# Optimization experiments

Measured on AMD Instinct MI355X. Metric: run time of the kernel, lower is better.

The kernel has to match this reference:

```python
import jax, jax.numpy as jnp
import numpy as np

B, T, U, N, K, H, O = 64, 800, 64, 64, 10, 512, 121
CLIP_LSTM, CLIP_OUT = 10.0, 100.0


def setup_inputs() -> dict:
    key = jax.random.key(0)
    ks = jax.random.split(key, 16)
    s = 0.08
    return {
        "strokes": jax.random.normal(ks[0], (B, T, 3), jnp.float32),
        "transcriptions": jax.random.uniform(ks[1], (B, U, N), jnp.float32),
        "W0": jax.random.normal(ks[2], (3 + N, 4 * H), jnp.float32) * s,
        "R0": jax.random.normal(ks[3], (H, 4 * H), jnp.float32) * s,
        "b0": jnp.zeros((4 * H,), jnp.float32),
        "Wd": jax.random.normal(ks[4], (H, 3 * K), jnp.float32) * 0.01,
        "bd": jnp.zeros((3 * K,), jnp.float32),
        "W1": jax.random.normal(ks[5], (H + N + 3, 4 * H), jnp.float32) * s,
        "R1": jax.random.normal(ks[6], (H, 4 * H), jnp.float32) * s,
        "b1": jnp.zeros((4 * H,), jnp.float32),
        "W2": jax.random.normal(ks[7], (H + N + 3, 4 * H), jnp.float32) * s,
        "R2": jax.random.normal(ks[8], (H, 4 * H), jnp.float32) * s,
        "b2": jnp.zeros((4 * H,), jnp.float32),
        "Wo": jax.random.normal(ks[9], (3 * H, O), jnp.float32) * s,
        "bo": jnp.zeros((O,), jnp.float32),
    }


def _lstm_step(h, c, z):
    i, f, g, o = jnp.split(z, 4, axis=-1)
    c2 = jax.nn.sigmoid(f) * c + jax.nn.sigmoid(i) * jnp.tanh(g)
    h2 = jax.nn.sigmoid(o) * jnp.tanh(c2)
    return h2, c2


def _lstm_layer(x_seq, W, R, b):
    # x_seq: [T, B, D] -> hidden sequence [T, B, H]
    xz = jnp.einsum('tbd,dh->tbh', x_seq, W) + b  # precompute input projections

    def step(carry, xz_t):
        h, c = carry
        h2, c2 = _lstm_step(h, c, xz_t + h @ R)
        return (h2, c2), h2

    z0 = jnp.zeros((x_seq.shape[1], R.shape[0]), x_seq.dtype)
    _, hs = jax.lax.scan(step, (z0, z0), xz)
    return hs


def _make_clipper(cv):
    @jax.custom_vjp
    def f(y):
        return y
    f.defvjp(lambda y: (y, None), lambda _, dy: (jnp.clip(dy, -cv, cv),))
    return f


_clip_lstm = _make_clipper(CLIP_LSTM)
_clip_out = _make_clipper(CLIP_OUT)


def _forward(strokes, transcriptions, W0, R0, b0, Wd, bd, W1, R1, b1, W2, R2, b2, Wo, bo):
    idx = jnp.arange(1, U + 2, dtype=strokes.dtype)  # enumerated char positions [U+1]
    x_t = jnp.swapaxes(strokes, 0, 1)  # [T, B, 3]

    def step(carry, x):
        w, kappa, h, c = carry
        z = jnp.concatenate([x, w], axis=-1) @ W0 + h @ R0 + b0
        h2, c2 = _lstm_step(h, c, z)
        y = jnp.exp(h2 @ Wd + bd).reshape(-1, 3, K)  # [B, 3, K]
        alpha, beta, dk = y[:, 0], y[:, 1], y[:, 2]
        kappa2 = kappa + dk  # [B, K]
        # Gaussian window over U+1 positions, summed over K mixtures
        phi = alpha[..., None] * jnp.exp(-beta[..., None] * (kappa2[..., None] - idx) ** 2)
        wfull = phi.sum(axis=1)  # [B, U+1]
        att = jnp.argmax(wfull, axis=-1).astype(strokes.dtype)  # [B]
        w2 = jnp.einsum('bu,bun->bn', wfull[:, :U], transcriptions)  # soft window [B, N]
        return (w2, kappa2, h2, c2), (h2, w2, att)

    zf = lambda d: jnp.zeros((B, d), strokes.dtype)
    init = (zf(N), zf(K), zf(H), zf(H))
    _, (h0_seq, w_seq, att_seq) = jax.lax.scan(step, init, x_t)

    x1 = jnp.concatenate([_clip_lstm(h0_seq), w_seq, x_t], axis=-1)  # [T, B, H+N+3]
    h1_seq = _lstm_layer(x1, W1, R1, b1)
    x2 = jnp.concatenate([_clip_lstm(h1_seq), w_seq, x_t], axis=-1)
    h2_seq = _lstm_layer(x2, W2, R2, b2)
    hall = jnp.concatenate([h0_seq, h1_seq, h2_seq], axis=-1)  # [T, B, 3H]
    out = _clip_out(hall @ Wo + bo)
    return jnp.swapaxes(out, 0, 1), jnp.swapaxes(att_seq, 0, 1)  # [B,T,O], [B,T]


def reference(strokes, transcriptions, W0, R0, b0, Wd, bd, W1, R1, b1, W2, R2, b2, Wo, bo):
    return _forward(strokes, transcriptions, W0, R0, b0, Wd, bd, W1, R1, b1, W2, R2, b2, Wo, bo)
```

## Files before the change

kernel.cpp:

```cpp
#include <hip/hip_runtime.h>

#define B_   64
#define T_   800
#define U_   64
#define N_   64
#define KMIX 10
#define H_   512
#define O_   121
#define C4_  2048

#define NB_L0  64
#define NB_L1  64
#define NB_L2  64
#define NB_OUT 8
#define NB_ATT 4
#define NBLK  (NB_L0 + NB_L1 + NB_L2 + NB_OUT + NB_ATT)
#define NTHR  1024
#define RING  8
#define RB    (RING - 1)
#define FS    8

#define AL(pp) __hip_atomic_load((pp), __ATOMIC_RELAXED, __HIP_MEMORY_SCOPE_AGENT)

struct Params {
  const float* strokes; const float* transcr;
  const float* W0; const float* b0;
  const float* bd;
  const float* W1; const float* b1;
  const float* W2; const float* b2;
  const float* bo;
  const float4* PR0; const float4* PW0w;
  const float4* PH1; const float4* PR1; const float4* PW1w;
  const float4* PH2; const float4* PR2; const float4* PW2w;
  const float4* PWo; const float4* PWd;
  float* h0r; float* h1r; float* h2r;
  float* wr;
  int *h0f, *h1f, *h2f, *wfl, *outf;
  float* outp; float* attp;
};

__device__ __forceinline__ float sigf(float x) { return 1.0f / (1.0f + expf(-x)); }

__device__ __forceinline__ double f32q(double x) {
  double ax = fabs(x);
  if (ax >= 0x1p-126) return (double)(float)x;
  return rint(x * 0x1p149) * 0x1p-149;
}

__device__ __forceinline__ void cstoref(float* p, float v) {
  __hip_atomic_store(p, v, __ATOMIC_RELAXED, __HIP_MEMORY_SCOPE_AGENT);
}

__device__ __forceinline__ int* FP(int* arr, int tt, int bq) {
  return arr + ((size_t)tt * 8 + bq) * FS;
}
__device__ __forceinline__ void waitflag(const int* f, int target) {
  while (__hip_atomic_load(f, __ATOMIC_RELAXED, __HIP_MEMORY_SCOPE_AGENT) < target)
    __builtin_amdgcn_s_sleep(1);
}
__device__ __forceinline__ void postflag(int* f) {
  __hip_atomic_fetch_add(f, 1, __ATOMIC_RELAXED, __HIP_MEMORY_SCOPE_AGENT);
}

__device__ __forceinline__ void stage4k(float* dstL, const float* src, int t) {
  const double* s = (const double*)src;
  double v0 = AL(s + t), v1 = AL(s + 1024 + t);
  double* d = (double*)dstL;
  d[t] = v0; d[1024 + t] = v1;
}
__device__ __forceinline__ void stage4k2(float* d1, const float* s1,
                                         float* d2, const float* s2, int t) {
  const double* a = (const double*)s1;
  const double* b = (const double*)s2;
  double a0 = AL(a + t), a1 = AL(a + 1024 + t);
  double b0 = AL(b + t), b1 = AL(b + 1024 + t);
  double* dA = (double*)d1; dA[t] = a0; dA[1024 + t] = a1;
  double* dB = (double*)d2; dB[t] = b0; dB[1024 + t] = b1;
}
__device__ __forceinline__ void stage512(float* dstL, const float* src, int t) {
  if (t < 256) {
    double v = AL((const double*)src + t);
    ((double*)dstL)[t] = v;
  }
}

__device__ __forceinline__ void dot4gl(const float* Xl,
                                       const float4* __restrict__ W,
                                       int k4, int col, float acc[4]) {
  const float4* X = (const float4*)Xl;
  #pragma unroll 2
  for (int kk = 0; kk < k4; ++kk) {
    float4 xv = X[kk];
    #pragma unroll
    for (int g = 0; g < 4; ++g) {
      float4 wv = W[kk * C4_ + g * H_ + col];
      acc[g] = fmaf(xv.x, wv.x, acc[g]);
      acc[g] = fmaf(xv.y, wv.y, acc[g]);
      acc[g] = fmaf(xv.z, wv.z, acc[g]);
      acc[g] = fmaf(xv.w, wv.w, acc[g]);
    }
  }
}

__device__ __forceinline__ float dot1l(const float* Xl,
                                       const float4* __restrict__ W,
                                       int k4, int stride) {
  const float4* X = (const float4*)Xl;
  float a = 0.0f;
  #pragma unroll 4
  for (int kk = 0; kk < k4; ++kk) {
    float4 xv = X[kk];
    float4 wv = W[kk * stride];
    a = fmaf(xv.x, wv.x, a); a = fmaf(xv.y, wv.y, a);
    a = fmaf(xv.z, wv.z, a); a = fmaf(xv.w, wv.w, a);
  }
  return a;
}

__global__ void pack_k(const float* __restrict__ src, float* __restrict__ dst,
                       int K, int C, int ld) {
  int idx = blockIdx.x * 256 + threadIdx.x;
  if (idx >= K * C) return;
  int k = idx / C, c = idx - k * C;
  dst[(size_t)(k >> 2) * C * 4 + (size_t)c * 4 + (k & 3)] = src[(size_t)k * ld + c];
}

__global__ __launch_bounds__(NTHR, 4)
void net_kernel(Params p) {
  const int q = blockIdx.x;
  const int t = threadIdx.x;

  __shared__ float  s_buf[12288];
  __shared__ float  s_y[16][32];
  __shared__ float  s_k2[16][10];
  __shared__ float  s_kap[16][10];
  __shared__ double s_wf[16][66];

  if (q < NB_L0) {
    const int bq = q >> 3, colg = q & 7;
    const int kh = t >> 9;
    const int bl = (t >> 6) & 7, cl = t & 63;
    const int b = bq * 8 + bl, col = colg * 64 + cl;
    float* sh = s_buf;
    float* sw = s_buf + 4096;
    float4* s_red = (float4*)(s_buf + 4608);
    float creg = 0.0f;
    for (int i = 0; i < T_; ++i) {
      if (t == 0) {
        if (i >= 1) waitflag(FP(p.h0f, i - 1, bq), 8);
        if (i >= 8) waitflag(FP(p.outf, i - 8, bq), 1);
      }
      __syncthreads();
      const int slp = (i - 1) & RB;
      stage4k(sh, &p.h0r[((size_t)slp * B_ + bq * 8) * H_], t);
      float acc[4] = {0.f, 0.f, 0.f, 0.f};
      if (kh == 0) {
        const float* xs = &p.strokes[(b * T_ + i) * 3];
        float x0 = xs[0], x1 = xs[1], x2 = xs[2];
        #pragma unroll
        for (int g = 0; g < 4; ++g) {
          int cg = g * H_ + col;
          acc[g] = p.b0[cg] + x0 * p.W0[cg] + x1 * p.W0[C4_ + cg] + x2 * p.W0[2 * C4_ + cg];
        }
      }
      __syncthreads();
      dot4gl(sh + bl * H_ + kh * 256, p.PR0 + (size_t)kh * 64 * C4_, 64, col, acc);
      if (t == 0 && i >= 1) waitflag(FP(p.wfl, i - 1, bq), 1);
      __syncthreads();
      stage512(sw, &p.wr[((size_t)slp * B_ + bq * 8) * N_], t);
      __syncthreads();
      dot4gl(sw + bl * N_ + kh * 32, p.PW0w + (size_t)kh * 8 * C4_, 8, col, acc);
      if (kh) { float4 r; r.x = acc[0]; r.y = acc[1]; r.z = acc[2]; r.w = acc[3]; s_red[t - 512] = r; }
      __syncthreads();
      if (!kh) {
        float4 r = s_red[t];
        float cn = sigf(acc[1] + r.y) * creg + sigf(acc[0] + r.x) * tanhf(acc[2] + r.z);
        float hn = sigf(acc[3] + r.w) * tanhf(cn);
        creg = cn;
        cstoref(&p.h0r[((size_t)(i & RB) * B_ + b) * H_ + col], hn);
      }
      __syncthreads();
      if (t == 0) postflag(FP(p.h0f, i, bq));
    }
  } else if (q < NB_L0 + NB_L1) {
    const int qq = q - NB_L0;
    const int bq = qq >> 3, colg = qq & 7;
    const int kh = t >> 9;
    const int bl = (t >> 6) & 7, cl = t & 63;
    const int b = bq * 8 + bl, col = colg * 64 + cl;
    float* sh0 = s_buf;
    float* sh1 = s_buf + 4096;
    float* sw  = s_buf + 8192;
    float4* s_red = (float4*)(s_buf + 8704);
    float creg = 0.0f;
    for (int tt = 0; tt < T_; ++tt) {
      if (t == 0) {
        waitflag(FP(p.h0f, tt, bq), 8);
        if (tt >= 1) waitflag(FP(p.h1f, tt - 1, bq), 8);
        if (tt >= 7) waitflag(FP(p.outf, tt - 7, bq), 1);
      }
      __syncthreads();
      const int sl = tt & RB, slp = (tt - 1) & RB;
      stage4k2(sh0, &p.h0r[((size_t)sl * B_ + bq * 8) * H_],
               sh1, &p.h1r[((size_t)slp * B_ + bq * 8) * H_], t);
      float acc[4] = {0.f, 0.f, 0.f, 0.f};
      if (kh == 0) {
        const float* xs = &p.strokes[(b * T_ + tt) * 3];
        float x0 = xs[0], x1 = xs[1], x2 = xs[2];
        #pragma unroll
        for (int g = 0; g < 4; ++g) {
          int cg = g * H_ + col;
          acc[g] = p.b1[cg] + x0 * p.W1[576 * C4_ + cg] + x1 * p.W1[577 * C4_ + cg]
                            + x2 * p.W1[578 * C4_ + cg];
        }
      }
      __syncthreads();
      dot4gl(sh0 + bl * H_ + kh * 256, p.PH1 + (size_t)kh * 64 * C4_, 64, col, acc);
      dot4gl(sh1 + bl * H_ + kh * 256, p.PR1 + (size_t)kh * 64 * C4_, 64, col, acc);
      if (t == 0) waitflag(FP(p.wfl, tt, bq), 1);
      __syncthreads();
      stage512(sw, &p.wr[((size_t)sl * B_ + bq * 8) * N_], t);
      __syncthreads();
      dot4gl(sw + bl * N_ + kh * 32, p.PW1w + (size_t)kh * 8 * C4_, 8, col, acc);
      if (kh) { float4 r; r.x = acc[0]; r.y = acc[1]; r.z = acc[2]; r.w = acc[3]; s_red[t - 512] = r; }
      __syncthreads();
      if (!kh) {
        float4 r = s_red[t];
        float cn = sigf(acc[1] + r.y) * creg + sigf(acc[0] + r.x) * tanhf(acc[2] + r.z);
        float hn = sigf(acc[3] + r.w) * tanhf(cn);
        creg = cn;
        cstoref(&p.h1r[((size_t)sl * B_ + b) * H_ + col], hn);
      }
      __syncthreads();
      if (t == 0) postflag(FP(p.h1f, tt, bq));
    }
  } else if (q < NB_L0 + NB_L1 + NB_L2) {
    const int qq = q - NB_L0 - NB_L1;
    const int bq = qq >> 3, colg = qq & 7;
    const int kh = t >> 9;
    const int bl = (t >> 6) & 7, cl = t & 63;
    const int b = bq * 8 + bl, col = colg * 64 + cl;
    float* sh1 = s_buf;
    float* sh2 = s_buf + 4096;
    float* sw  = s_buf + 8192;
    float4* s_red = (float4*)(s_buf + 8704);
    float creg = 0.0f;
    for (int tt = 0; tt < T_; ++tt) {
      if (t == 0) {
        waitflag(FP(p.h1f, tt, bq), 8);
        waitflag(FP(p.wfl, tt, bq), 1);
        if (tt >= 1) waitflag(FP(p.h2f, tt - 1, bq), 8);
        if (tt >= 6) waitflag(FP(p.outf, tt - 6, bq), 1);
      }
      __syncthreads();
      const int sl = tt & RB, slp = (tt - 1) & RB;
      stage4k2(sh1, &p.h1r[((size_t)sl * B_ + bq * 8) * H_],
               sh2, &p.h2r[((size_t)slp * B_ + bq * 8) * H_], t);
      stage512(sw, &p.wr[((size_t)sl * B_ + bq * 8) * N_], t);
      float acc[4] = {0.f, 0.f, 0.f, 0.f};
      if (kh == 0) {
        const float* xs = &p.strokes[(b * T_ + tt) * 3];
        float x0 = xs[0], x1 = xs[1], x2 = xs[2];
        #pragma unroll
        for (int g = 0; g < 4; ++g) {
          int cg = g * H_ + col;
          acc[g] = p.b2[cg] + x0 * p.W2[576 * C4_ + cg] + x1 * p.W2[577 * C4_ + cg]
                            + x2 * p.W2[578 * C4_ + cg];
        }
      }
      __syncthreads();
      dot4gl(sh1 + bl * H_ + kh * 256, p.PH2 + (size_t)kh * 64 * C4_, 64, col, acc);
      dot4gl(sw + bl * N_ + kh * 32, p.PW2w + (size_t)kh * 8 * C4_, 8, col, acc);
      dot4gl(sh2 + bl * H_ + kh * 256, p.PR2 + (size_t)kh * 64 * C4_, 64, col, acc);
      if (kh) { float4 r; r.x = acc[0]; r.y = acc[1]; r.z = acc[2]; r.w = acc[3]; s_red[t - 512] = r; }
      __syncthreads();
      if (!kh) {
        float4 r = s_red[t];
        float cn = sigf(acc[1] + r.y) * creg + sigf(acc[0] + r.x) * tanhf(acc[2] + r.z);
        float hn = sigf(acc[3] + r.w) * tanhf(cn);
        creg = cn;
        cstoref(&p.h2r[((size_t)sl * B_ + b) * H_ + col], hn);
      }
      __syncthreads();
      if (t == 0) postflag(FP(p.h2f, tt, bq));
    }
  } else if (q < NB_L0 + NB_L1 + NB_L2 + NB_OUT) {
    const int bq = q - NB_L0 - NB_L1 - NB_L2;
    const int kh = t >> 9;
    const int bl = (t >> 6) & 7, ol = t & 63;
    const int b = bq * 8 + bl;
    const int oo1 = ol;
    const bool v2 = (ol < O_ - 64);
    const int oo2 = v2 ? (ol + 64) : 0;
    float* sx0 = s_buf;
    float* sx1 = s_buf + 4096;
    float* sx2 = s_buf + 8192;
    float* s_red = (float*)s_wf;
    for (int tt = 0; tt < T_; ++tt) {
      if (t == 0) {
        waitflag(FP(p.h0f, tt, bq), 8);
        waitflag(FP(p.h1f, tt, bq), 8);
        waitflag(FP(p.h2f, tt, bq), 8);
      }
      __syncthreads();
      const int sl = tt & RB;
      {
        const double* a = (const double*)&p.h0r[((size_t)sl * B_ + bq * 8) * H_];
        const double* c = (const double*)&p.h1r[((size_t)sl * B_ + bq * 8) * H_];
        const double* e = (const double*)&p.h2r[((size_t)sl * B_ + bq * 8) * H_];
        double a0 = AL(a + t), a1 = AL(a + 1024 + t);
        double c0 = AL(c + t), c1 = AL(c + 1024 + t);
        double e0 = AL(e + t), e1 = AL(e + 1024 + t);
        double* dA = (double*)sx0; dA[t] = a0; dA[1024 + t] = a1;
        double* dC = (double*)sx1; dC[t] = c0; dC[1024 + t] = c1;
        double* dE = (double*)sx2; dE[t] = e0; dE[1024 + t] = e1;
      }
      __syncthreads();
      const float* X0 = sx0 + bl * H_ + kh * 256;
      const float* X1 = sx1 + bl * H_ + kh * 256;
      const float* X2 = sx2 + bl * H_ + kh * 256;
      const size_t khO = (size_t)(kh * 64) * O_;
      float a1v = kh ? 0.0f : p.bo[oo1];
      a1v += dot1l(X0, p.PWo + khO + oo1, 64, O_);
      a1v += dot1l(X1, p.PWo + (size_t)128 * O_ + khO + oo1, 64, O_);
      a1v += dot1l(X2, p.PWo + (size_t)256 * O_ + khO + oo1, 64, O_);
      float a2v = kh ? 0.0f : p.bo[oo2];
      a2v += dot1l(X0, p.PWo + khO + oo2, 64, O_);
      a2v += dot1l(X1, p.PWo + (size_t)128 * O_ + khO + oo2, 64, O_);
      a2v += dot1l(X2, p.PWo + (size_t)256 * O_ + khO + oo2, 64, O_);
      if (kh) { s_red[(t - 512) * 2] = a1v; s_red[(t - 512) * 2 + 1] = a2v; }
      __syncthreads();
      if (!kh) {
        a1v += s_red[t * 2];
        a2v += s_red[t * 2 + 1];
        __builtin_nontemporal_store(a1v, &p.outp[(size_t)(b * T_ + tt) * O_ + oo1]);
        if (v2) __builtin_nontemporal_store(a2v, &p.outp[(size_t)(b * T_ + tt) * O_ + oo2]);
      }
      __syncthreads();
      if (t == 0) postflag(FP(p.outf, tt, bq));
    }
  } else {
    const int qa = q - NB_L0 - NB_L1 - NB_L2 - NB_OUT;
    const int lb = t >> 5, s = t & 31;
    const int ub = qa * 16 + lb;
    for (int z = t; z < 160; z += NTHR) ((float*)s_kap)[z] = 0.0f;
    __syncthreads();
    for (int tt = 0; tt < T_; ++tt) {
      if (t == 0) {
        waitflag(FP(p.h0f, tt, 2 * qa), 8);
        waitflag(FP(p.h0f, tt, 2 * qa + 1), 8);
      }
      __syncthreads();
      const int sl = tt & RB;
      {
        const double* sA = (const double*)&p.h0r[((size_t)sl * B_ + qa * 16) * H_];
        double v[4];
        #pragma unroll
        for (int k = 0; k < 4; ++k) v[k] = AL(sA + k * 1024 + t);
        double* d = (double*)s_buf;
        #pragma unroll
        for (int k = 0; k < 4; ++k) d[k * 1024 + t] = v[k];
      }
      __syncthreads();
      if (t < 512 && s < 30) {
        float a = p.bd[s] + dot1l(s_buf + lb * H_, p.PWd + s, 128, 30);
        float y = expf(a);
        s_y[lb][s] = y;
        if (s >= 20) {
          float k2 = s_kap[lb][s - 20] + y;
          s_kap[lb][s - 20] = k2;
          s_k2[lb][s - 20] = k2;
        }
      }
      __syncthreads();
      if (t < 512) {
        for (int u = s; u < U_ + 1; u += 32) {
          double wf = 0.0;
          #pragma unroll
          for (int k = 0; k < KMIX; ++k) {
            float d32 = s_k2[lb][k] - (float)(u + 1);
            float sq  = d32 * d32;
            float m   = -(s_y[lb][10 + k] * sq);
            double e  = exp((double)m);
            double e32 = (e < 0x1p-126) ? 0.0 : (double)(float)e;
            wf += f32q((double)s_y[lb][k] * e32);
          }
          s_wf[lb][u] = wf;
        }
      }
      __syncthreads();
      if (t < 512 && s == 0) {
        int am = 0; double bv = s_wf[lb][0];
        for (int u = 1; u < U_ + 1; ++u) {
          double v = s_wf[lb][u];
          if (v > bv) { bv = v; am = u; }
        }
        __builtin_nontemporal_store((float)am, &p.attp[ub * T_ + tt]);
      }
      if (t < 512) {
        for (int n = s; n < N_; n += 32) {
          float a2 = 0.f;
          for (int u = 0; u < U_; ++u)
            a2 = fmaf((float)s_wf[lb][u], p.transcr[(size_t)(ub * U_ + u) * N_ + n], a2);
          cstoref(&p.wr[((size_t)sl * B_ + ub) * N_ + n], a2);
        }
      }
      __syncthreads();
      if (t == 0) {
        postflag(FP(p.wfl, tt, 2 * qa));
        postflag(FP(p.wfl, tt, 2 * qa + 1));
      }
    }
  }
}

extern "C" void kernel_launch(void* const* d_in, const int* in_sizes, int n_in,
                              void* d_out, int out_size, void* d_ws, size_t ws_size,
                              hipStream_t stream) {
  (void)in_sizes; (void)n_in; (void)out_size; (void)ws_size;
  const float* strokes = (const float*)d_in[0];
  const float* transcr = (const float*)d_in[1];
  const float* W0 = (const float*)d_in[2];
  const float* R0 = (const float*)d_in[3];
  const float* b0 = (const float*)d_in[4];
  const float* Wd = (const float*)d_in[5];
  const float* bd = (const float*)d_in[6];
  const float* W1 = (const float*)d_in[7];
  const float* R1 = (const float*)d_in[8];
  const float* b1 = (const float*)d_in[9];
  const float* W2 = (const float*)d_in[10];
  const float* R2 = (const float*)d_in[11];
  const float* b2 = (const float*)d_in[12];
  const float* Wo = (const float*)d_in[13];
  const float* bo = (const float*)d_in[14];

  float* ws = (float*)d_ws;
  size_t off = 0;
  float* h0r = ws + off; off += (size_t)RING * B_ * H_;
  float* h1r = ws + off; off += (size_t)RING * B_ * H_;
  float* h2r = ws + off; off += (size_t)RING * B_ * H_;
  float* wr  = ws + off; off += (size_t)RING * B_ * N_;
  const size_t FLAGN = (size_t)T_ * 8 * FS;
  int* h0f  = (int*)(ws + off); off += FLAGN;
  int* h1f  = (int*)(ws + off); off += FLAGN;
  int* h2f  = (int*)(ws + off); off += FLAGN;
  int* wfl  = (int*)(ws + off); off += FLAGN;
  int* outf = (int*)(ws + off); off += FLAGN;
  size_t stateFloats = off;
  float* PR0  = ws + off; off += (size_t)512 * 2048;
  float* PW0w = ws + off; off += (size_t)64 * 2048;
  float* PH1  = ws + off; off += (size_t)512 * 2048;
  float* PR1  = ws + off; off += (size_t)512 * 2048;
  float* PW1w = ws + off; off += (size_t)64 * 2048;
  float* PH2  = ws + off; off += (size_t)512 * 2048;
  float* PR2  = ws + off; off += (size_t)512 * 2048;
  float* PW2w = ws + off; off += (size_t)64 * 2048;
  float* PWo  = ws + off; off += (size_t)1536 * 121;
  float* PWd  = ws + off; off += (size_t)512 * 30;

  (void)hipMemsetAsync(d_ws, 0, stateFloats * sizeof(float), stream);

  auto packl = [&](const float* src, float* dst, int K, int C, int ld) {
    int n = K * C;
    pack_k<<<dim3((n + 255) / 256), dim3(256), 0, stream>>>(src, dst, K, C, ld);
  };
  packl(R0, PR0, 512, 2048, 2048);
  packl(W0 + 3 * 2048, PW0w, 64, 2048, 2048);
  packl(W1, PH1, 512, 2048, 2048);
  packl(R1, PR1, 512, 2048, 2048);
  packl(W1 + 512 * 2048, PW1w, 64, 2048, 2048);
  packl(W2, PH2, 512, 2048, 2048);
  packl(R2, PR2, 512, 2048, 2048);
  packl(W2 + 512 * 2048, PW2w, 64, 2048, 2048);
  packl(Wo, PWo, 1536, 121, 121);
  packl(Wd, PWd, 512, 30, 30);

  Params p;
  p.strokes = strokes; p.transcr = transcr;
  p.W0 = W0; p.b0 = b0; p.bd = bd;
  p.W1 = W1; p.b1 = b1; p.W2 = W2; p.b2 = b2; p.bo = bo;
  p.PR0 = (const float4*)PR0; p.PW0w = (const float4*)PW0w;
  p.PH1 = (const float4*)PH1; p.PR1 = (const float4*)PR1; p.PW1w = (const float4*)PW1w;
  p.PH2 = (const float4*)PH2; p.PR2 = (const float4*)PR2; p.PW2w = (const float4*)PW2w;
  p.PWo = (const float4*)PWo; p.PWd = (const float4*)PWd;
  p.h0r = h0r; p.h1r = h1r; p.h2r = h2r; p.wr = wr;
  p.h0f = h0f; p.h1f = h1f; p.h2f = h2f; p.wfl = wfl; p.outf = outf;
  p.outp = (float*)d_out;
  p.attp = (float*)d_out + (size_t)B_ * T_ * O_;

  void* args[] = { (void*)&p };
  (void)hipLaunchCooperativeKernel((const void*)net_kernel, dim3(NBLK), dim3(NTHR),
                                   args, 0, stream);
}
```

Measured before the change: 52.89 ms.

## Reuse each weight load across eight batch rows in LSTM recurrent blocks

The LSTM recurrent blocks now give each thread one gate column across all 8 batch rows, with the K dimension split four ways. Each float4 weight load is reused for 8 FMAs instead of 1, and partial sums are reduced through shared memory before the gate nonlinearity. This cuts global/L2 weight traffic per step, at the cost of more LDS reads of hidden state and an extra reduction pass. The attention block also spreads its window and soft-window work over all 1024 threads and posts the window flag before the argmax, so downstream layers can start sooner.

```diff
diff --git a/kernel.cpp b/kernel.cpp
--- a/kernel.cpp
+++ b/kernel.cpp
@@ -84,20 +84,21 @@
   }
 }
 
-__device__ __forceinline__ void dot4gl(const float* Xl,
-                                       const float4* __restrict__ W,
-                                       int k4, int col, float acc[4]) {
-  const float4* X = (const float4*)Xl;
-  #pragma unroll 2
-  for (int kk = 0; kk < k4; ++kk) {
-    float4 xv = X[kk];
+__device__ __forceinline__ void dotb8(const float4* __restrict__ X, int xld4,
+                                      const float4* __restrict__ Wg,
+                                      int kk0, int niter, float acc[8]) {
+  const float4* Wp = Wg + (size_t)kk0 * C4_;
+  #pragma unroll 8
+  for (int i = 0; i < niter; ++i) {
+    float4 wv = Wp[(size_t)i * C4_];
+    const int kk = kk0 + i;
     #pragma unroll
-    for (int g = 0; g < 4; ++g) {
-      float4 wv = W[kk * C4_ + g * H_ + col];
-      acc[g] = fmaf(xv.x, wv.x, acc[g]);
-      acc[g] = fmaf(xv.y, wv.y, acc[g]);
-      acc[g] = fmaf(xv.z, wv.z, acc[g]);
-      acc[g] = fmaf(xv.w, wv.w, acc[g]);
+    for (int b = 0; b < 8; ++b) {
+      float4 xv = X[b * xld4 + kk];
+      acc[b] = fmaf(xv.x, wv.x, acc[b]);
+      acc[b] = fmaf(xv.y, wv.y, acc[b]);
+      acc[b] = fmaf(xv.z, wv.z, acc[b]);
+      acc[b] = fmaf(xv.w, wv.w, acc[b]);
     }
   }
 }
@@ -138,12 +139,13 @@
 
   if (q < NB_L0) {
     const int bq = q >> 3, colg = q & 7;
-    const int kh = t >> 9;
-    const int bl = (t >> 6) & 7, cl = t & 63;
-    const int b = bq * 8 + bl, col = colg * 64 + cl;
+    const int kq = t >> 8, g = (t >> 6) & 3, cl = t & 63;
+    const int col = colg * 64 + cl;
     float* sh = s_buf;
     float* sw = s_buf + 4096;
-    float4* s_red = (float4*)(s_buf + 4608);
+    float* sp = s_buf;
+    const float4* WgR = p.PR0 + (size_t)g * H_ + col;
+    const float4* WgW = p.PW0w + (size_t)g * H_ + col;
     float creg = 0.0f;
     for (int i = 0; i < T_; ++i) {
       if (t == 0) {
@@ -153,31 +155,39 @@
       __syncthreads();
       const int slp = (i - 1) & RB;
       stage4k(sh, &p.h0r[((size_t)slp * B_ + bq * 8) * H_], t);
-      float acc[4] = {0.f, 0.f, 0.f, 0.f};
-      if (kh == 0) {
+      __syncthreads();
+      float acc[8] = {0,0,0,0,0,0,0,0};
+      dotb8((const float4*)sh, 128, WgR, kq * 32, 32, acc);
+      if (t == 0 && i >= 1) waitflag(FP(p.wfl, i - 1, bq), 1);
+      __syncthreads();
+      stage512(sw, &p.wr[((size_t)slp * B_ + bq * 8) * N_], t);
+      __syncthreads();
+      dotb8((const float4*)sw, 16, WgW, kq * 4, 4, acc);
+      __syncthreads();
+      #pragma unroll
+      for (int b = 0; b < 8; ++b)
+        sp[((kq * 4 + g) * 8 + b) * 64 + cl] = acc[b];
+      __syncthreads();
+      if (t < 512) {
+        const int bl = t >> 6, cl2 = t & 63;
+        const int b = bq * 8 + bl;
+        const int col2 = colg * 64 + cl2;
         const float* xs = &p.strokes[(b * T_ + i) * 3];
         float x0 = xs[0], x1 = xs[1], x2 = xs[2];
+        float z[4];
         #pragma unroll
-        for (int g = 0; g < 4; ++g) {
-          int cg = g * H_ + col;
-          acc[g] = p.b0[cg] + x0 * p.W0[cg] + x1 * p.W0[C4_ + cg] + x2 * p.W0[2 * C4_ + cg];
+        for (int g2 = 0; g2 < 4; ++g2) {
+          int cg = g2 * H_ + col2;
+          float v = p.b0[cg] + x0 * p.W0[cg] + x1 * p.W0[C4_ + cg] + x2 * p.W0[2 * C4_ + cg];
+          #pragma unroll
+          for (int kq2 = 0; kq2 < 4; ++kq2)
+            v += sp[((kq2 * 4 + g2) * 8 + bl) * 64 + cl2];
+          z[g2] = v;
         }
-      }
-      __syncthreads();
-      dot4gl(sh + bl * H_ + kh * 256, p.PR0 + (size_t)kh * 64 * C4_, 64, col, acc);
-      if (t == 0 && i >= 1) waitflag(FP(p.wfl, i - 1, bq), 1);
-      __syncthreads();
-      stage512(sw, &p.wr[((size_t)slp * B_ + bq * 8) * N_], t);
-      __syncthreads();
-      dot4gl(sw + bl * N_ + kh * 32, p.PW0w + (size_t)kh * 8 * C4_, 8, col, acc);
-      if (kh) { float4 r; r.x = acc[0]; r.y = acc[1]; r.z = acc[2]; r.w = acc[3]; s_red[t - 512] = r; }
-      __syncthreads();
-      if (!kh) {
-        float4 r = s_red[t];
-        float cn = sigf(acc[1] + r.y) * creg + sigf(acc[0] + r.x) * tanhf(acc[2] + r.z);
-        float hn = sigf(acc[3] + r.w) * tanhf(cn);
+        float cn = sigf(z[1]) * creg + sigf(z[0]) * tanhf(z[2]);
+        float hn = sigf(z[3]) * tanhf(cn);
         creg = cn;
-        cstoref(&p.h0r[((size_t)(i & RB) * B_ + b) * H_ + col], hn);
+        cstoref(&p.h0r[((size_t)(i & RB) * B_ + b) * H_ + col2], hn);
       }
       __syncthreads();
       if (t == 0) postflag(FP(p.h0f, i, bq));
@@ -185,13 +195,15 @@
   } else if (q < NB_L0 + NB_L1) {
     const int qq = q - NB_L0;
     const int bq = qq >> 3, colg = qq & 7;
-    const int kh = t >> 9;
-    const int bl = (t >> 6) & 7, cl = t & 63;
-    const int b = bq * 8 + bl, col = colg * 64 + cl;
+    const int kq = t >> 8, g = (t >> 6) & 3, cl = t & 63;
+    const int col = colg * 64 + cl;
     float* sh0 = s_buf;
     float* sh1 = s_buf + 4096;
     float* sw  = s_buf + 8192;
-    float4* s_red = (float4*)(s_buf + 8704);
+    float* sp  = s_buf;
+    const float4* WgH = p.PH1 + (size_t)g * H_ + col;
+    const float4* WgR = p.PR1 + (size_t)g * H_ + col;
+    const float4* WgW = p.PW1w + (size_t)g * H_ + col;
     float creg = 0.0f;
     for (int tt = 0; tt < T_; ++tt) {
       if (t == 0) {
@@ -203,33 +215,41 @@
       const int sl = tt & RB, slp = (tt - 1) & RB;
       stage4k2(sh0, &p.h0r[((size_t)sl * B_ + bq * 8) * H_],
                sh1, &p.h1r[((size_t)slp * B_ + bq * 8) * H_], t);
-      float acc[4] = {0.f, 0.f, 0.f, 0.f};
-      if (kh == 0) {
+      __syncthreads();
+      float acc[8] = {0,0,0,0,0,0,0,0};
+      dotb8((const float4*)sh0, 128, WgH, kq * 32, 32, acc);
+      dotb8((const float4*)sh1, 128, WgR, kq * 32, 32, acc);
+      if (t == 0) waitflag(FP(p.wfl, tt, bq), 1);
+      __syncthreads();
+      stage512(sw, &p.wr[((size_t)sl * B_ + bq * 8) * N_], t);
+      __syncthreads();
+      dotb8((const float4*)sw, 16, WgW, kq * 4, 4, acc);
+      __syncthreads();
+      #pragma unroll
+      for (int b = 0; b < 8; ++b)
+        sp[((kq * 4 + g) * 8 + b) * 64 + cl] = acc[b];
+      __syncthreads();
+      if (t < 512) {
+        const int bl = t >> 6, cl2 = t & 63;
+        const int b = bq * 8 + bl;
+        const int col2 = colg * 64 + cl2;
         const float* xs = &p.strokes[(b * T_ + tt) * 3];
         float x0 = xs[0], x1 = xs[1], x2 = xs[2];
+        float z[4];
         #pragma unroll
-        for (int g = 0; g < 4; ++g) {
-          int cg = g * H_ + col;
-          acc[g] = p.b1[cg] + x0 * p.W1[576 * C4_ + cg] + x1 * p.W1[577 * C4_ + cg]
-                            + x2 * p.W1[578 * C4_ + cg];
+        for (int g2 = 0; g2 < 4; ++g2) {
+          int cg = g2 * H_ + col2;
+          float v = p.b1[cg] + x0 * p.W1[576 * C4_ + cg] + x1 * p.W1[577 * C4_ + cg]
+                             + x2 * p.W1[578 * C4_ + cg];
+          #pragma unroll
+          for (int kq2 = 0; kq2 < 4; ++kq2)
+            v += sp[((kq2 * 4 + g2) * 8 + bl) * 64 + cl2];
+          z[g2] = v;
         }
-      }
-      __syncthreads();
-      dot4gl(sh0 + bl * H_ + kh * 256, p.PH1 + (size_t)kh * 64 * C4_, 64, col, acc);
-      dot4gl(sh1 + bl * H_ + kh * 256, p.PR1 + (size_t)kh * 64 * C4_, 64, col, acc);
-      if (t == 0) waitflag(FP(p.wfl, tt, bq), 1);
-      __syncthreads();
-      stage512(sw, &p.wr[((size_t)sl * B_ + bq * 8) * N_], t);
-      __syncthreads();
-      dot4gl(sw + bl * N_ + kh * 32, p.PW1w + (size_t)kh * 8 * C4_, 8, col, acc);
-      if (kh) { float4 r; r.x = acc[0]; r.y = acc[1]; r.z = acc[2]; r.w = acc[3]; s_red[t - 512] = r; }
-      __syncthreads();
-      if (!kh) {
-        float4 r = s_red[t];
-        float cn = sigf(acc[1] + r.y) * creg + sigf(acc[0] + r.x) * tanhf(acc[2] + r.z);
-        float hn = sigf(acc[3] + r.w) * tanhf(cn);
+        float cn = sigf(z[1]) * creg + sigf(z[0]) * tanhf(z[2]);
+        float hn = sigf(z[3]) * tanhf(cn);
         creg = cn;
-        cstoref(&p.h1r[((size_t)sl * B_ + b) * H_ + col], hn);
+        cstoref(&p.h1r[((size_t)sl * B_ + b) * H_ + col2], hn);
       }
       __syncthreads();
       if (t == 0) postflag(FP(p.h1f, tt, bq));
@@ -237,13 +257,15 @@
   } else if (q < NB_L0 + NB_L1 + NB_L2) {
     const int qq = q - NB_L0 - NB_L1;
     const int bq = qq >> 3, colg = qq & 7;
-    const int kh = t >> 9;
-    const int bl = (t >> 6) & 7, cl = t & 63;
-    const int b = bq * 8 + bl, col = colg * 64 + cl;
+    const int kq = t >> 8, g = (t >> 6) & 3, cl = t & 63;
+    const int col = colg * 64 + cl;
     float* sh1 = s_buf;
     float* sh2 = s_buf + 4096;
     float* sw  = s_buf + 8192;
-    float4* s_red = (float4*)(s_buf + 8704);
+    float* sp  = s_buf;
+    const float4* WgH = p.PH2 + (size_t)g * H_ + col;
+    const float4* WgR = p.PR2 + (size_t)g * H_ + col;
+    const float4* WgW = p.PW2w + (size_t)g * H_ + col;
     float creg = 0.0f;
     for (int tt = 0; tt < T_; ++tt) {
       if (t == 0) {
@@ -257,29 +279,37 @@
       stage4k2(sh1, &p.h1r[((size_t)sl * B_ + bq * 8) * H_],
                sh2, &p.h2r[((size_t)slp * B_ + bq * 8) * H_], t);
       stage512(sw, &p.wr[((size_t)sl * B_ + bq * 8) * N_], t);
-      float acc[4] = {0.f, 0.f, 0.f, 0.f};
-      if (kh == 0) {
+      __syncthreads();
+      float acc[8] = {0,0,0,0,0,0,0,0};
+      dotb8((const float4*)sh1, 128, WgH, kq * 32, 32, acc);
+      dotb8((const float4*)sw, 16, WgW, kq * 4, 4, acc);
+      dotb8((const float4*)sh2, 128, WgR, kq * 32, 32, acc);
+      __syncthreads();
+      #pragma unroll
+      for (int b = 0; b < 8; ++b)
+        sp[((kq * 4 + g) * 8 + b) * 64 + cl] = acc[b];
+      __syncthreads();
+      if (t < 512) {
+        const int bl = t >> 6, cl2 = t & 63;
+        const int b = bq * 8 + bl;
+        const int col2 = colg * 64 + cl2;
         const float* xs = &p.strokes[(b * T_ + tt) * 3];
         float x0 = xs[0], x1 = xs[1], x2 = xs[2];
+        float z[4];
         #pragma unroll
-        for (int g = 0; g < 4; ++g) {
-          int cg = g * H_ + col;
-          acc[g] = p.b2[cg] + x0 * p.W2[576 * C4_ + cg] + x1 * p.W2[577 * C4_ + cg]
-                            + x2 * p.W2[578 * C4_ + cg];
+        for (int g2 = 0; g2 < 4; ++g2) {
+          int cg = g2 * H_ + col2;
+          float v = p.b2[cg] + x0 * p.W2[576 * C4_ + cg] + x1 * p.W2[577 * C4_ + cg]
+                             + x2 * p.W2[578 * C4_ + cg];
+          #pragma unroll
+          for (int kq2 = 0; kq2 < 4; ++kq2)
+            v += sp[((kq2 * 4 + g2) * 8 + bl) * 64 + cl2];
+          z[g2] = v;
         }
-      }
-      __syncthreads();
-      dot4gl(sh1 + bl * H_ + kh * 256, p.PH2 + (size_t)kh * 64 * C4_, 64, col, acc);
-      dot4gl(sw + bl * N_ + kh * 32, p.PW2w + (size_t)kh * 8 * C4_, 8, col, acc);
-      dot4gl(sh2 + bl * H_ + kh * 256, p.PR2 + (size_t)kh * 64 * C4_, 64, col, acc);
-      if (kh) { float4 r; r.x = acc[0]; r.y = acc[1]; r.z = acc[2]; r.w = acc[3]; s_red[t - 512] = r; }
-      __syncthreads();
-      if (!kh) {
-        float4 r = s_red[t];
-        float cn = sigf(acc[1] + r.y) * creg + sigf(acc[0] + r.x) * tanhf(acc[2] + r.z);
-        float hn = sigf(acc[3] + r.w) * tanhf(cn);
+        float cn = sigf(z[1]) * creg + sigf(z[0]) * tanhf(z[2]);
+        float hn = sigf(z[3]) * tanhf(cn);
         creg = cn;
-        cstoref(&p.h2r[((size_t)sl * B_ + b) * H_ + col], hn);
+        cstoref(&p.h2r[((size_t)sl * B_ + b) * H_ + col2], hn);
       }
       __syncthreads();
       if (t == 0) postflag(FP(p.h2f, tt, bq));
@@ -341,7 +371,8 @@
     }
   } else {
     const int qa = q - NB_L0 - NB_L1 - NB_L2 - NB_OUT;
-    const int lb = t >> 5, s = t & 31;
+    const int lb = (t >> 5) & 15, s = t & 31;
+    const int ss = s | ((t >> 4) & 32);
     const int ub = qa * 16 + lb;
     for (int z = t; z < 160; z += NTHR) ((float*)s_kap)[z] = 0.0f;
     __syncthreads();
@@ -373,22 +404,32 @@
         }
       }
       __syncthreads();
-      if (t < 512) {
-        for (int u = s; u < U_ + 1; u += 32) {
-          double wf = 0.0;
-          #pragma unroll
-          for (int k = 0; k < KMIX; ++k) {
-            float d32 = s_k2[lb][k] - (float)(u + 1);
-            float sq  = d32 * d32;
-            float m   = -(s_y[lb][10 + k] * sq);
-            double e  = exp((double)m);
-            double e32 = (e < 0x1p-126) ? 0.0 : (double)(float)e;
-            wf += f32q((double)s_y[lb][k] * e32);
-          }
-          s_wf[lb][u] = wf;
+      for (int u = ss; u < U_ + 1; u += 64) {
+        double wf = 0.0;
+        #pragma unroll
+        for (int k = 0; k < KMIX; ++k) {
+          float d32 = s_k2[lb][k] - (float)(u + 1);
+          float sq  = d32 * d32;
+          float m   = -(s_y[lb][10 + k] * sq);
+          double e  = exp((double)m);
+          double e32 = (e < 0x1p-126) ? 0.0 : (double)(float)e;
+          wf += f32q((double)s_y[lb][k] * e32);
         }
-      }
-      __syncthreads();
+        s_wf[lb][u] = wf;
+      }
+      __syncthreads();
+      {
+        const int n = ss;
+        float a2 = 0.f;
+        for (int u = 0; u < U_; ++u)
+          a2 = fmaf((float)s_wf[lb][u], p.transcr[(size_t)(ub * U_ + u) * N_ + n], a2);
+        cstoref(&p.wr[((size_t)sl * B_ + ub) * N_ + n], a2);
+      }
+      __syncthreads();
+      if (t == 0) {
+        postflag(FP(p.wfl, tt, 2 * qa));
+        postflag(FP(p.wfl, tt, 2 * qa + 1));
+      }
       if (t < 512 && s == 0) {
         int am = 0; double bv = s_wf[lb][0];
         for (int u = 1; u < U_ + 1; ++u) {
@@ -396,19 +437,6 @@
           if (v > bv) { bv = v; am = u; }
         }
         __builtin_nontemporal_store((float)am, &p.attp[ub * T_ + tt]);
-      }
-      if (t < 512) {
-        for (int n = s; n < N_; n += 32) {
-          float a2 = 0.f;
-          for (int u = 0; u < U_; ++u)
-            a2 = fmaf((float)s_wf[lb][u], p.transcr[(size_t)(ub * U_ + u) * N_ + n], a2);
-          cstoref(&p.wr[((size_t)sl * B_ + ub) * N_ + n], a2);
-        }
-      }
-      __syncthreads();
-      if (t == 0) {
-        postflag(FP(p.wfl, tt, 2 * qa));
-        postflag(FP(p.wfl, tt, 2 * qa + 1));
       }
     }
   }
```

New measurement: 63.25 ms. 1.2x slower.

## Replace block barriers with per-wave flag posting and all-thread spin waits

Applied to the files above, without the earlier changes.

Each wave that writes hidden-state outputs now posts its own progress flag after a waitcnt, so consumer targets rise from 8 to 64 and the trailing __syncthreads plus single-thread post are gone. All threads spin on the flags directly instead of thread 0 waiting and then a barrier. The output block posts its consumption flag right after staging rather than after computing. The attention stage moves to 8 blocks covering 8 batch rows each, with one thread per position and per output column, and these blocks also post per wave. The aim is to shorten the per-timestep critical path across the pipelined layers, at the cost of more atomic traffic and heavier polling, with a risk of memory-ordering subtleties.

```diff
diff --git a/kernel.cpp b/kernel.cpp
--- a/kernel.cpp
+++ b/kernel.cpp
@@ -13,7 +13,7 @@
 #define NB_L1  64
 #define NB_L2  64
 #define NB_OUT 8
-#define NB_ATT 4
+#define NB_ATT 8
 #define NBLK  (NB_L0 + NB_L1 + NB_L2 + NB_OUT + NB_ATT)
 #define NTHR  1024
 #define RING  8
@@ -61,6 +61,10 @@
 __device__ __forceinline__ void postflag(int* f) {
   __hip_atomic_fetch_add(f, 1, __ATOMIC_RELAXED, __HIP_MEMORY_SCOPE_AGENT);
 }
+__device__ __forceinline__ void postflag_w(int* f) {
+  __builtin_amdgcn_s_waitcnt(0);
+  __hip_atomic_fetch_add(f, 1, __ATOMIC_RELAXED, __HIP_MEMORY_SCOPE_AGENT);
+}
 
 __device__ __forceinline__ void stage4k(float* dstL, const float* src, int t) {
   const double* s = (const double*)src;
@@ -131,10 +135,10 @@
   const int t = threadIdx.x;
 
   __shared__ float  s_buf[12288];
-  __shared__ float  s_y[16][32];
-  __shared__ float  s_k2[16][10];
-  __shared__ float  s_kap[16][10];
-  __shared__ double s_wf[16][66];
+  __shared__ float  s_y[8][32];
+  __shared__ float  s_k2[8][10];
+  __shared__ float  s_kap[8][10];
+  __shared__ double s_wf[8][66];
 
   if (q < NB_L0) {
     const int bq = q >> 3, colg = q & 7;
@@ -146,11 +150,8 @@
     float4* s_red = (float4*)(s_buf + 4608);
     float creg = 0.0f;
     for (int i = 0; i < T_; ++i) {
-      if (t == 0) {
-        if (i >= 1) waitflag(FP(p.h0f, i - 1, bq), 8);
-        if (i >= 8) waitflag(FP(p.outf, i - 8, bq), 1);
-      }
-      __syncthreads();
+      if (i >= 1) waitflag(FP(p.h0f, i - 1, bq), 64);
+      if (i >= 8) waitflag(FP(p.outf, i - 8, bq), 1);
       const int slp = (i - 1) & RB;
       stage4k(sh, &p.h0r[((size_t)slp * B_ + bq * 8) * H_], t);
       float acc[4] = {0.f, 0.f, 0.f, 0.f};
@@ -165,8 +166,7 @@
       }
       __syncthreads();
       dot4gl(sh + bl * H_ + kh * 256, p.PR0 + (size_t)kh * 64 * C4_, 64, col, acc);
-      if (t == 0 && i >= 1) waitflag(FP(p.wfl, i - 1, bq), 1);
-      __syncthreads();
+      if (i >= 1) waitflag(FP(p.wfl, i - 1, bq), 8);
       stage512(sw, &p.wr[((size_t)slp * B_ + bq * 8) * N_], t);
       __syncthreads();
       dot4gl(sw + bl * N_ + kh * 32, p.PW0w + (size_t)kh * 8 * C4_, 8, col, acc);
@@ -178,9 +178,8 @@
         float hn = sigf(acc[3] + r.w) * tanhf(cn);
         creg = cn;
         cstoref(&p.h0r[((size_t)(i & RB) * B_ + b) * H_ + col], hn);
-      }
-      __syncthreads();
-      if (t == 0) postflag(FP(p.h0f, i, bq));
+        if (cl == 0) postflag_w(FP(p.h0f, i, bq));
+      }
     }
   } else if (q < NB_L0 + NB_L1) {
     const int qq = q - NB_L0;
@@ -194,12 +193,9 @@
     float4* s_red = (float4*)(s_buf + 8704);
     float creg = 0.0f;
     for (int tt = 0; tt < T_; ++tt) {
-      if (t == 0) {
-        waitflag(FP(p.h0f, tt, bq), 8);
-        if (tt >= 1) waitflag(FP(p.h1f, tt - 1, bq), 8);
-        if (tt >= 7) waitflag(FP(p.outf, tt - 7, bq), 1);
-      }
-      __syncthreads();
+      if (tt >= 1) waitflag(FP(p.h1f, tt - 1, bq), 64);
+      waitflag(FP(p.h0f, tt, bq), 64);
+      if (tt >= 7) waitflag(FP(p.outf, tt - 7, bq), 1);
       const int sl = tt & RB, slp = (tt - 1) & RB;
       stage4k2(sh0, &p.h0r[((size_t)sl * B_ + bq * 8) * H_],
                sh1, &p.h1r[((size_t)slp * B_ + bq * 8) * H_], t);
@@ -217,8 +213,7 @@
       __syncthreads();
       dot4gl(sh0 + bl * H_ + kh * 256, p.PH1 + (size_t)kh * 64 * C4_, 64, col, acc);
       dot4gl(sh1 + bl * H_ + kh * 256, p.PR1 + (size_t)kh * 64 * C4_, 64, col, acc);
-      if (t == 0) waitflag(FP(p.wfl, tt, bq), 1);
-      __syncthreads();
+      waitflag(FP(p.wfl, tt, bq), 8);
       stage512(sw, &p.wr[((size_t)sl * B_ + bq * 8) * N_], t);
       __syncthreads();
       dot4gl(sw + bl * N_ + kh * 32, p.PW1w + (size_t)kh * 8 * C4_, 8, col, acc);
@@ -230,9 +225,8 @@
         float hn = sigf(acc[3] + r.w) * tanhf(cn);
         creg = cn;
         cstoref(&p.h1r[((size_t)sl * B_ + b) * H_ + col], hn);
-      }
-      __syncthreads();
-      if (t == 0) postflag(FP(p.h1f, tt, bq));
+        if (cl == 0) postflag_w(FP(p.h1f, tt, bq));
+      }
     }
   } else if (q < NB_L0 + NB_L1 + NB_L2) {
     const int qq = q - NB_L0 - NB_L1;
@@ -246,13 +240,10 @@
     float4* s_red = (float4*)(s_buf + 8704);
     float creg = 0.0f;
     for (int tt = 0; tt < T_; ++tt) {
-      if (t == 0) {
-        waitflag(FP(p.h1f, tt, bq), 8);
-        waitflag(FP(p.wfl, tt, bq), 1);
-        if (tt >= 1) waitflag(FP(p.h2f, tt - 1, bq), 8);
-        if (tt >= 6) waitflag(FP(p.outf, tt - 6, bq), 1);
-      }
-      __syncthreads();
+      if (tt >= 1) waitflag(FP(p.h2f, tt - 1, bq), 64);
+      waitflag(FP(p.h1f, tt, bq), 64);
+      waitflag(FP(p.wfl, tt, bq), 8);
+      if (tt >= 6) waitflag(FP(p.outf, tt - 6, bq), 1);
       const int sl = tt & RB, slp = (tt - 1) & RB;
       stage4k2(sh1, &p.h1r[((size_t)sl * B_ + bq * 8) * H_],
                sh2, &p.h2r[((size_t)slp * B_ + bq * 8) * H_], t);
@@ -280,9 +271,8 @@
         float hn = sigf(acc[3] + r.w) * tanhf(cn);
         creg = cn;
         cstoref(&p.h2r[((size_t)sl * B_ + b) * H_ + col], hn);
-      }
-      __syncthreads();
-      if (t == 0) postflag(FP(p.h2f, tt, bq));
+        if (cl == 0) postflag_w(FP(p.h2f, tt, bq));
+      }
     }
   } else if (q < NB_L0 + NB_L1 + NB_L2 + NB_OUT) {
     const int bq = q - NB_L0 - NB_L1 - NB_L2;
@@ -297,12 +287,9 @@
     float* sx2 = s_buf + 8192;
     float* s_red = (float*)s_wf;
     for (int tt = 0; tt < T_; ++tt) {
-      if (t == 0) {
-        waitflag(FP(p.h0f, tt, bq), 8);
-        waitflag(FP(p.h1f, tt, bq), 8);
-        waitflag(FP(p.h2f, tt, bq), 8);
-      }
-      __syncthreads();
+      waitflag(FP(p.h0f, tt, bq), 64);
+      waitflag(FP(p.h1f, tt, bq), 64);
+      waitflag(FP(p.h2f, tt, bq), 64);
       const int sl = tt & RB;
       {
         const double* a = (const double*)&p.h0r[((size_t)sl * B_ + bq * 8) * H_];
@@ -316,6 +303,7 @@
         double* dE = (double*)sx2; dE[t] = e0; dE[1024 + t] = e1;
       }
       __syncthreads();
+      if (t == 0) postflag(FP(p.outf, tt, bq));
       const float* X0 = sx0 + bl * H_ + kh * 256;
       const float* X1 = sx1 + bl * H_ + kh * 256;
       const float* X2 = sx2 + bl * H_ + kh * 256;
@@ -336,33 +324,24 @@
         __builtin_nontemporal_store(a1v, &p.outp[(size_t)(b * T_ + tt) * O_ + oo1]);
         if (v2) __builtin_nontemporal_store(a2v, &p.outp[(size_t)(b * T_ + tt) * O_ + oo2]);
       }
-      __syncthreads();
-      if (t == 0) postflag(FP(p.outf, tt, bq));
     }
   } else {
-    const int qa = q - NB_L0 - NB_L1 - NB_L2 - NB_OUT;
-    const int lb = t >> 5, s = t & 31;
-    const int ub = qa * 16 + lb;
-    for (int z = t; z < 160; z += NTHR) ((float*)s_kap)[z] = 0.0f;
+    const int bq = q - NB_L0 - NB_L1 - NB_L2 - NB_OUT;
+    const int lb = t >> 7, s = t & 127;
+    const int ub = bq * 8 + lb;
+    for (int z = t; z < 80; z += NTHR) ((float*)s_kap)[z] = 0.0f;
     __syncthreads();
     for (int tt = 0; tt < T_; ++tt) {
-      if (t == 0) {
-        waitflag(FP(p.h0f, tt, 2 * qa), 8);
-        waitflag(FP(p.h0f, tt, 2 * qa + 1), 8);
-      }
-      __syncthreads();
+      waitflag(FP(p.h0f, tt, bq), 64);
       const int sl = tt & RB;
       {
-        const double* sA = (const double*)&p.h0r[((size_t)sl * B_ + qa * 16) * H_];
-        double v[4];
-        #pragma unroll
-        for (int k = 0; k < 4; ++k) v[k] = AL(sA + k * 1024 + t);
+        const double* sA = (const double*)&p.h0r[((size_t)sl * B_ + bq * 8) * H_];
+        double v0 = AL(sA + t), v1 = AL(sA + 1024 + t);
         double* d = (double*)s_buf;
-        #pragma unroll
-        for (int k = 0; k < 4; ++k) d[k * 1024 + t] = v[k];
-      }
-      __syncthreads();
-      if (t < 512 && s < 30) {
+        d[t] = v0; d[1024 + t] = v1;
+      }
+      __syncthreads();
+      if (s < 30) {
         float a = p.bd[s] + dot1l(s_buf + lb * H_, p.PWd + s, 128, 30);
         float y = expf(a);
         s_y[lb][s] = y;
@@ -373,42 +352,35 @@
         }
       }
       __syncthreads();
-      if (t < 512) {
-        for (int u = s; u < U_ + 1; u += 32) {
-          double wf = 0.0;
-          #pragma unroll
-          for (int k = 0; k < KMIX; ++k) {
-            float d32 = s_k2[lb][k] - (float)(u + 1);
-            float sq  = d32 * d32;
-            float m   = -(s_y[lb][10 + k] * sq);
-            double e  = exp((double)m);
-            double e32 = (e < 0x1p-126) ? 0.0 : (double)(float)e;
-            wf += f32q((double)s_y[lb][k] * e32);
-          }
-          s_wf[lb][u] = wf;
-        }
-      }
-      __syncthreads();
-      if (t < 512 && s == 0) {
+      if (s < U_ + 1) {
+        const int u = s;
+        double wf = 0.0;
+        #pragma unroll
+        for (int k = 0; k < KMIX; ++k) {
+          float d32 = s_k2[lb][k] - (float)(u + 1);
+          float sq  = d32 * d32;
+          float m   = -(s_y[lb][10 + k] * sq);
+          double e  = exp((double)m);
+          double e32 = (e < 0x1p-126) ? 0.0 : (double)(float)e;
+          wf += f32q((double)s_y[lb][k] * e32);
+        }
+        s_wf[lb][u] = wf;
+      }
+      __syncthreads();
+      if (s < N_) {
+        float a2 = 0.f;
+        for (int u = 0; u < U_; ++u)
+          a2 = fmaf((float)s_wf[lb][u], p.transcr[(size_t)(ub * U_ + u) * N_ + s], a2);
+        cstoref(&p.wr[((size_t)sl * B_ + ub) * N_ + s], a2);
+      }
+      if ((t & 127) == 0) postflag_w(FP(p.wfl, tt, bq));
+      if (s == 127) {
         int am = 0; double bv = s_wf[lb][0];
         for (int u = 1; u < U_ + 1; ++u) {
           double v = s_wf[lb][u];
           if (v > bv) { bv = v; am = u; }
         }
         __builtin_nontemporal_store((float)am, &p.attp[ub * T_ + tt]);
-      }
-      if (t < 512) {
-        for (int n = s; n < N_; n += 32) {
-          float a2 = 0.f;
-          for (int u = 0; u < U_; ++u)
-            a2 = fmaf((float)s_wf[lb][u], p.transcr[(size_t)(ub * U_ + u) * N_ + n], a2);
-          cstoref(&p.wr[((size_t)sl * B_ + ub) * N_ + n], a2);
-        }
-      }
-      __syncthreads();
-      if (t == 0) {
-        postflag(FP(p.wfl, tt, 2 * qa));
-        postflag(FP(p.wfl, tt, 2 * qa + 1));
       }
     }
   }
```

Result: slower. 76.24 ms (+44.2%).

## Spread attention window over more blocks and transpose transcriptions for vector loads

Applied to the files above, without the earlier changes.

Doubles the number of attention blocks so each handles 8 batch rows with 128 threads per row, which lets each thread compute one window position instead of looping. The transcription tensor is transposed once per launch so the soft-window dot product can use contiguous float4 loads. The wait and post flags are reduced to one per block, and the completion flag is now posted before the argmax. This shortens the serial per-timestep attention stage that layer 0 depends on, at the cost of four more resident blocks and an extra pack kernel.

```diff
diff --git a/kernel.cpp b/kernel.cpp
--- a/kernel.cpp
+++ b/kernel.cpp
@@ -13,7 +13,7 @@
 #define NB_L1  64
 #define NB_L2  64
 #define NB_OUT 8
-#define NB_ATT 4
+#define NB_ATT 8
 #define NBLK  (NB_L0 + NB_L1 + NB_L2 + NB_OUT + NB_ATT)
 #define NTHR  1024
 #define RING  8
@@ -24,6 +24,7 @@
 
 struct Params {
   const float* strokes; const float* transcr;
+  const float* transcrT;
   const float* W0; const float* b0;
   const float* bd;
   const float* W1; const float* b1;
@@ -123,6 +124,14 @@
   if (idx >= K * C) return;
   int k = idx / C, c = idx - k * C;
   dst[(size_t)(k >> 2) * C * 4 + (size_t)c * 4 + (k & 3)] = src[(size_t)k * ld + c];
+}
+
+__global__ void pack_t(const float* __restrict__ src, float* __restrict__ dst) {
+  int idx = blockIdx.x * 256 + threadIdx.x;
+  if (idx >= B_ * U_ * N_) return;
+  int b = idx >> 12, r = idx & 4095;
+  int u = r >> 6, n = r & 63;
+  dst[((size_t)b * N_ + n) * U_ + u] = src[((size_t)b * U_ + u) * N_ + n];
 }
 
 __global__ __launch_bounds__(NTHR, 4)
@@ -340,29 +349,23 @@
       if (t == 0) postflag(FP(p.outf, tt, bq));
     }
   } else {
-    const int qa = q - NB_L0 - NB_L1 - NB_L2 - NB_OUT;
-    const int lb = t >> 5, s = t & 31;
-    const int ub = qa * 16 + lb;
-    for (int z = t; z < 160; z += NTHR) ((float*)s_kap)[z] = 0.0f;
+    const int bq = q - NB_L0 - NB_L1 - NB_L2 - NB_OUT;
+    const int lb = t >> 7, s = t & 127;
+    const int ub = bq * 8 + lb;
+    for (int z = t; z < 80; z += NTHR) ((float*)s_kap)[z] = 0.0f;
     __syncthreads();
     for (int tt = 0; tt < T_; ++tt) {
-      if (t == 0) {
-        waitflag(FP(p.h0f, tt, 2 * qa), 8);
-        waitflag(FP(p.h0f, tt, 2 * qa + 1), 8);
-      }
+      if (t == 0) waitflag(FP(p.h0f, tt, bq), 8);
       __syncthreads();
       const int sl = tt & RB;
       {
-        const double* sA = (const double*)&p.h0r[((size_t)sl * B_ + qa * 16) * H_];
-        double v[4];
-        #pragma unroll
-        for (int k = 0; k < 4; ++k) v[k] = AL(sA + k * 1024 + t);
+        const double* sA = (const double*)&p.h0r[((size_t)sl * B_ + bq * 8) * H_];
+        double v0 = AL(sA + t), v1 = AL(sA + 1024 + t);
         double* d = (double*)s_buf;
-        #pragma unroll
-        for (int k = 0; k < 4; ++k) d[k * 1024 + t] = v[k];
-      }
-      __syncthreads();
-      if (t < 512 && s < 30) {
+        d[t] = v0; d[1024 + t] = v1;
+      }
+      __syncthreads();
+      if (s < 30) {
         float a = p.bd[s] + dot1l(s_buf + lb * H_, p.PWd + s, 128, 30);
         float y = expf(a);
         s_y[lb][s] = y;
@@ -373,42 +376,43 @@
         }
       }
       __syncthreads();
-      if (t < 512) {
-        for (int u = s; u < U_ + 1; u += 32) {
-          double wf = 0.0;
-          #pragma unroll
-          for (int k = 0; k < KMIX; ++k) {
-            float d32 = s_k2[lb][k] - (float)(u + 1);
-            float sq  = d32 * d32;
-            float m   = -(s_y[lb][10 + k] * sq);
-            double e  = exp((double)m);
-            double e32 = (e < 0x1p-126) ? 0.0 : (double)(float)e;
-            wf += f32q((double)s_y[lb][k] * e32);
-          }
-          s_wf[lb][u] = wf;
-        }
-      }
-      __syncthreads();
-      if (t < 512 && s == 0) {
+      if (s < U_ + 1) {
+        const int u = s;
+        double wf = 0.0;
+        #pragma unroll
+        for (int k = 0; k < KMIX; ++k) {
+          float d32 = s_k2[lb][k] - (float)(u + 1);
+          float sq  = d32 * d32;
+          float m   = -(s_y[lb][10 + k] * sq);
+          double e  = exp((double)m);
+          double e32 = (e < 0x1p-126) ? 0.0 : (double)(float)e;
+          wf += f32q((double)s_y[lb][k] * e32);
+        }
+        s_wf[lb][u] = wf;
+      }
+      __syncthreads();
+      if (s < N_) {
+        const float4* Tp = (const float4*)&p.transcrT[((size_t)ub * N_ + s) * U_];
+        float a2 = 0.f;
+        #pragma unroll
+        for (int kk = 0; kk < 16; ++kk) {
+          float4 tv = Tp[kk];
+          a2 = fmaf((float)s_wf[lb][4 * kk],     tv.x, a2);
+          a2 = fmaf((float)s_wf[lb][4 * kk + 1], tv.y, a2);
+          a2 = fmaf((float)s_wf[lb][4 * kk + 2], tv.z, a2);
+          a2 = fmaf((float)s_wf[lb][4 * kk + 3], tv.w, a2);
+        }
+        cstoref(&p.wr[((size_t)sl * B_ + ub) * N_ + s], a2);
+      }
+      __syncthreads();
+      if (t == 0) postflag(FP(p.wfl, tt, bq));
+      if (s == 127) {
         int am = 0; double bv = s_wf[lb][0];
         for (int u = 1; u < U_ + 1; ++u) {
           double v = s_wf[lb][u];
           if (v > bv) { bv = v; am = u; }
         }
         __builtin_nontemporal_store((float)am, &p.attp[ub * T_ + tt]);
-      }
-      if (t < 512) {
-        for (int n = s; n < N_; n += 32) {
-          float a2 = 0.f;
-          for (int u = 0; u < U_; ++u)
-            a2 = fmaf((float)s_wf[lb][u], p.transcr[(size_t)(ub * U_ + u) * N_ + n], a2);
-          cstoref(&p.wr[((size_t)sl * B_ + ub) * N_ + n], a2);
-        }
-      }
-      __syncthreads();
-      if (t == 0) {
-        postflag(FP(p.wfl, tt, 2 * qa));
-        postflag(FP(p.wfl, tt, 2 * qa + 1));
       }
     }
   }
@@ -457,6 +461,7 @@
   float* PW2w = ws + off; off += (size_t)64 * 2048;
   float* PWo  = ws + off; off += (size_t)1536 * 121;
   float* PWd  = ws + off; off += (size_t)512 * 30;
+  float* TT   = ws + off; off += (size_t)B_ * U_ * N_;
 
   (void)hipMemsetAsync(d_ws, 0, stateFloats * sizeof(float), stream);
 
@@ -474,9 +479,10 @@
   packl(W2 + 512 * 2048, PW2w, 64, 2048, 2048);
   packl(Wo, PWo, 1536, 121, 121);
   packl(Wd, PWd, 512, 30, 30);
+  pack_t<<<dim3((B_ * U_ * N_ + 255) / 256), dim3(256), 0, stream>>>(transcr, TT);
 
   Params p;
-  p.strokes = strokes; p.transcr = transcr;
+  p.strokes = strokes; p.transcr = transcr; p.transcrT = TT;
   p.W0 = W0; p.b0 = b0; p.bd = bd;
   p.W1 = W1; p.b1 = b1; p.W2 = W2; p.b2 = b2; p.bo = bo;
   p.PR0 = (const float4*)PR0; p.PW0w = (const float4*)PW0w;
```

After: 52.81 ms. About the same (-0.1%).
